# Optimization experiments

Hardware: AMD Instinct MI355X
Metric: run time of the kernel (lower is better)

Reference implementation:

```python
import jax, jax.numpy as jnp
import numpy as np

PATCHES = 196
HEADS = 12


def build_attention_mask(patches, memory_tokens_list, extension=False):
    """Additive mask: masked entries -inf, allowed entries 0. Shape (1, Sq, Skv)."""
    class_tokens = len(memory_tokens_list) + 1
    input_tokens = patches + class_tokens
    total_tokens = input_tokens + sum(memory_tokens_list)
    mask = np.zeros((1, input_tokens, total_tokens), dtype=np.float32)
    mask[:, :, patches + 1:] = -np.inf
    prev = 0
    for i, mtok in enumerate(memory_tokens_list):
        ct = patches + 1 + i
        ms = input_tokens + prev
        me = ms + mtok
        if extension:
            mask[:, ct:, ct] = 0.0
            mask[:, ct:, ms:me] = 0.0
        else:
            mask[:, ct, ct] = 0.0
            mask[:, ct, ms:me] = 0.0
        prev += mtok
    return mask


def setup_inputs() -> dict:
    key = jax.random.key(0)
    ks = jax.random.split(key, 5)
    B, Sq, D, M = 64, PATCHES + 2, 768, 8  # 1 base class token + 1 memory class token
    std = 0.02
    return {
        "hidden_states": jax.random.normal(ks[0], (B, Sq, D), jnp.float32),
        "memory": jax.random.normal(ks[1], (1, M, D), jnp.float32) * std,
        "Wq": jax.random.normal(ks[2], (D, D), jnp.float32) * std,
        "bq": jnp.zeros((D,), jnp.float32),
        "Wk": jax.random.normal(ks[3], (D, D), jnp.float32) * std,
        "bk": jnp.zeros((D,), jnp.float32),
        "Wv": jax.random.normal(ks[4], (D, D), jnp.float32) * std,
        "bv": jnp.zeros((D,), jnp.float32),
    }


def _split_heads(x, heads):
    B, S, D = x.shape
    return x.reshape(B, S, heads, D // heads)  # bshd


def reference(hidden_states, memory, Wq, bq, Wk, bk, Wv, bv):
    B, Sq, D = hidden_states.shape
    M = memory.shape[1]
    head_dim = D // HEADS
    scale = 1.0 / jnp.sqrt(jnp.asarray(head_dim, hidden_states.dtype))
    # static additive mask (1, Sq, Skv)
    mask = jnp.asarray(build_attention_mask(PATCHES, [M]))

    with_memory = jnp.concatenate(
        [hidden_states, jnp.broadcast_to(memory, (B, M, D))], axis=1)  # (B, Skv, D)

    q = _split_heads(hidden_states @ Wq + bq, HEADS)  # (B,Sq,H,dh)
    k = _split_heads(with_memory @ Wk + bk, HEADS)    # (B,Skv,H,dh)
    v = _split_heads(with_memory @ Wv + bv, HEADS)

    scores = jnp.einsum("bqhd,bkhd->bhqk", q, k) * scale + mask[:, None]  # (B,H,Sq,Skv)
    probs = jax.nn.softmax(scores, axis=-1)  # dropout is identity in eval
    ctx = jnp.einsum("bhqk,bkhd->bqhd", probs, v)
    return ctx.reshape(B, Sq, D)
```

## Files before the change

### kernel.cpp

```cpp
#include <hip/hip_runtime.h>

typedef __attribute__((ext_vector_type(8))) short bf16x8;
typedef __attribute__((ext_vector_type(4))) float f32x4;
typedef __attribute__((ext_vector_type(4))) unsigned int u32x4;

#define NB 64
#define SQ 198
#define SKV 206
#define DM 768
#define NH 12
#define NROWS (NB * SKV)
#define NCOL 2304

static __device__ __forceinline__ unsigned short f2b(float f) {
  union { float f; unsigned u; } v; v.f = f;
  unsigned r = v.u + 0x7FFFu + ((v.u >> 16) & 1u);
  return (unsigned short)(r >> 16);
}

typedef const __attribute__((address_space(1))) unsigned int g_u32;
typedef __attribute__((address_space(3))) unsigned int l_u32;
static __device__ __forceinline__ void gload_lds16(const void* g, void* l) {
  __builtin_amdgcn_global_load_lds((g_u32*)g, (l_u32*)l, 16, 0, 0);
}

__global__ __launch_bounds__(256) void k_conv_x(const float* __restrict__ hid,
                                                const float* __restrict__ mem,
                                                unsigned short* __restrict__ xkv) {
  int idx = (blockIdx.x * 256 + threadIdx.x) * 8;
  int r = idx / DM;
  int c = idx - r * DM;
  int b = r / SKV, s = r - b * SKV;
  const float* src = (s < SQ) ? (hid + (b * SQ + s) * DM + c)
                              : (mem + (s - SQ) * DM + c);
  float4 v0 = ((const float4*)src)[0];
  float4 v1 = ((const float4*)src)[1];
  unsigned w0 = f2b(v0.x) | ((unsigned)f2b(v0.y) << 16);
  unsigned w1 = f2b(v0.z) | ((unsigned)f2b(v0.w) << 16);
  unsigned w2 = f2b(v1.x) | ((unsigned)f2b(v1.y) << 16);
  unsigned w3 = f2b(v1.z) | ((unsigned)f2b(v1.w) << 16);
  u32x4 o = {w0, w1, w2, w3};
  *(u32x4*)(xkv + idx) = o;
}

__global__ __launch_bounds__(256) void k_conv_w(const float* __restrict__ Wq,
                                                const float* __restrict__ Wk,
                                                const float* __restrict__ Wv,
                                                unsigned short* __restrict__ wt) {
  __shared__ float L[64][65];
  int w = blockIdx.z;
  int n0 = blockIdx.x * 64, k0 = blockIdx.y * 64;
  const float* W = (w == 0) ? Wq : (w == 1) ? Wk : Wv;
  int tid = threadIdx.x;
#pragma unroll
  for (int i = 0; i < 16; ++i) {
    int idx = i * 256 + tid;
    int lr = idx >> 6, lc = idx & 63;
    L[lr][lc] = W[(k0 + lr) * DM + n0 + lc];
  }
  __syncthreads();
  unsigned short* dst = wt + w * DM * DM;
#pragma unroll
  for (int o = 0; o < 2; ++o) {
    int gi = o * 256 + tid;
    int rn = gi >> 3, g = gi & 7;
    unsigned wrd[4];
#pragma unroll
    for (int jj = 0; jj < 4; ++jj) {
      float f0 = L[g * 8 + jj * 2 + 0][rn];
      float f1 = L[g * 8 + jj * 2 + 1][rn];
      wrd[jj] = f2b(f0) | ((unsigned)f2b(f1) << 16);
    }
    u32x4 o4 = {wrd[0], wrd[1], wrd[2], wrd[3]};
    *(u32x4*)(dst + (n0 + rn) * DM + k0 + g * 8) = o4;
  }
}

__global__ __launch_bounds__(256, 2) void k_gemm(const unsigned short* __restrict__ xkv,
                                                 const unsigned short* __restrict__ wt,
                                                 const float* __restrict__ bq,
                                                 const float* __restrict__ bk,
                                                 const float* __restrict__ bv,
                                                 unsigned short* __restrict__ cout) {
  __shared__ __align__(16) unsigned char smem[34816];
  int nt = blockIdx.x, mt = blockIdx.y;
  int row0 = mt * 128, col0 = nt * 128;
  int w = nt / 6;
  int colw0 = col0 - w * 768;
  int tid = threadIdx.x, lane = tid & 63, wid = tid >> 6;
  int wr = wid >> 1, wc = wid & 1;
  const unsigned short* wbase = wt + w * DM * DM;

  f32x4 zero = {0.f, 0.f, 0.f, 0.f};
  f32x4 acc[4][4];
#pragma unroll
  for (int i = 0; i < 4; ++i)
#pragma unroll
    for (int j = 0; j < 4; ++j) acc[i][j] = zero;

  const unsigned short* aSrc[4];
  const unsigned short* bSrc[4];
#pragma unroll
  for (int j = 0; j < 4; ++j) {
    int s = (wid * 4 + j) * 64 + lane;
    int r = s >> 3, g = s & 7;
    int gsrc = g ^ (r & 7);
    aSrc[j] = xkv   + (row0 + r)  * DM + gsrc * 8;
    bSrc[j] = wbase + (colw0 + r) * DM + gsrc * 8;
  }

  for (int ks = 0; ks < 12; ++ks) {
    int k0 = ks * 64;
    if (ks) __syncthreads();
#pragma unroll
    for (int j = 0; j < 4; ++j) {
      gload_lds16(aSrc[j] + k0, smem + (wid * 4 + j) * 1024);
      gload_lds16(bSrc[j] + k0, smem + 16384 + (wid * 4 + j) * 1024);
    }
    __syncthreads();
#pragma unroll
    for (int kk = 0; kk < 2; ++kk) {
      bf16x8 a[4], b[4];
      int kbyte = (kk * 32 + ((lane >> 4) * 8)) * 2;
#pragma unroll
      for (int mi = 0; mi < 4; ++mi) {
        int rr = wr * 64 + mi * 16 + (lane & 15);
        a[mi] = *(const bf16x8*)(smem + ((rr * 128 + kbyte) ^ ((rr & 7) << 4)));
      }
#pragma unroll
      for (int ni = 0; ni < 4; ++ni) {
        int rr = wc * 64 + ni * 16 + (lane & 15);
        b[ni] = *(const bf16x8*)(smem + 16384 + ((rr * 128 + kbyte) ^ ((rr & 7) << 4)));
      }
#pragma unroll
      for (int mi = 0; mi < 4; ++mi)
#pragma unroll
        for (int ni = 0; ni < 4; ++ni)
          acc[mi][ni] = __builtin_amdgcn_mfma_f32_16x16x32_bf16(a[mi], b[ni], acc[mi][ni], 0, 0, 0);
    }
  }

  const float* bias = (w == 0) ? bq : (w == 1) ? bk : bv;
  float bb[4];
#pragma unroll
  for (int ni = 0; ni < 4; ++ni) bb[ni] = bias[colw0 + wc * 64 + ni * 16 + (lane & 15)];

  __syncthreads();
#pragma unroll
  for (int mi = 0; mi < 4; ++mi)
#pragma unroll
    for (int ni = 0; ni < 4; ++ni)
#pragma unroll
      for (int r = 0; r < 4; ++r) {
        int row = wr * 64 + mi * 16 + (lane >> 4) * 4 + r;
        int col = wc * 64 + ni * 16 + (lane & 15);
        *(unsigned short*)(smem + row * 272 + col * 2) = f2b(acc[mi][ni][r] + bb[ni]);
      }
  __syncthreads();
#pragma unroll
  for (int it = 0; it < 8; ++it) {
    int gi = it * 256 + tid;
    int row = gi >> 4, g = gi & 15;
    u32x4 v = *(const u32x4*)(smem + row * 272 + g * 16);
    *(u32x4*)(cout + (row0 + row) * NCOL + col0 + g * 8) = v;
  }
}

static __device__ __forceinline__ int vt_off(int row, int col) {
  return row * 416 + ((col * 2) ^ (((row >> 3) & 1) << 4));
}

__global__ __launch_bounds__(256, 3) void k_attn(const unsigned short* __restrict__ cqkv,
                                                 float* __restrict__ out) {
  __shared__ __align__(16) unsigned short Ksh[208 * 64];
  __shared__ __align__(16) unsigned char  VtB[64 * 416];
  int bh = blockIdx.x;
  int b = bh / NH, h = bh - b * NH;
  int tid = threadIdx.x, lane = tid & 63, wid = tid >> 6;
  int g = lane >> 4, l = lane & 15;
  const unsigned short* Cb = cqkv + (b * SKV) * NCOL + h * 64;

  if (tid < 64) *(unsigned*)(VtB + vt_off(tid, 206)) = 0u;
  for (int i = tid; i < 208 * 8; i += 256) {
    int row = i >> 3, gg = i & 7;
    int srow = (row < SKV) ? row : (SKV - 1);
    u32x4 v = *(const u32x4*)(Cb + srow * NCOL + 768 + gg * 8);
    *(u32x4*)((unsigned char*)Ksh + ((row * 128 + gg * 16) ^ ((row & 7) << 4))) = v;
  }
  for (int i = tid; i < 206 * 8; i += 256) {
    int key = i >> 3, gg = i & 7;
    u32x4 v = *(const u32x4*)(Cb + key * NCOL + 1536 + gg * 8);
    union { u32x4 v4; unsigned short e[8]; } u; u.v4 = v;
#pragma unroll
    for (int j = 0; j < 8; ++j)
      *(unsigned short*)(VtB + vt_off(gg * 8 + j, key)) = u.e[j];
  }
  __syncthreads();

  const float scale = 0.125f;
  f32x4 zero4 = {0.f, 0.f, 0.f, 0.f};
  int srcA = ((g & 1) << 5) + l;
  int srcB = srcA + 16;
  bool hiHalf = (g >= 2);

  for (int qt = wid; qt < 13; qt += 4) {
    int qr = qt * 16 + l;
    int qld = qr > 197 ? 197 : qr;
    const unsigned short* qp = Cb + qld * NCOL + g * 8;
    bf16x8 qa0 = *(const bf16x8*)qp;
    bf16x8 qa1 = *(const bf16x8*)(qp + 32);

    f32x4 sc[13];
#pragma unroll
    for (int nt = 0; nt < 13; ++nt) sc[nt] = zero4;
#pragma unroll
    for (int nt = 0; nt < 13; ++nt) {
      int key = nt * 16 + l;
      int rb = key * 128, sw = (key & 7) << 4, kb = g * 16;
      bf16x8 kb0 = *(const bf16x8*)((const unsigned char*)Ksh + rb + (kb ^ sw));
      bf16x8 kb1 = *(const bf16x8*)((const unsigned char*)Ksh + rb + ((kb + 64) ^ sw));
      sc[nt] = __builtin_amdgcn_mfma_f32_16x16x32_bf16(kb0, qa0, sc[nt], 0, 0, 0);
      sc[nt] = __builtin_amdgcn_mfma_f32_16x16x32_bf16(kb1, qa1, sc[nt], 0, 0, 0);
    }

    float mx = -1e30f;
#pragma unroll
    for (int nt = 0; nt < 13; ++nt)
#pragma unroll
      for (int r = 0; r < 4; ++r) {
        int key = nt * 16 + g * 4 + r;
        float s = sc[nt][r] * scale;
        bool ok = (key < 197 || qr == 197) && (key < SKV);
        s = ok ? s : -1e30f;
        sc[nt][r] = s;
        mx = fmaxf(mx, s);
      }
    mx = fmaxf(mx, __shfl_xor(mx, 16));
    mx = fmaxf(mx, __shfl_xor(mx, 32));
    float sum = 0.f;
#pragma unroll
    for (int nt = 0; nt < 13; ++nt)
#pragma unroll
      for (int r = 0; r < 4; ++r) {
        float p = __expf(sc[nt][r] - mx);
        sc[nt][r] = p;
        sum += p;
      }
    sum += __shfl_xor(sum, 16);
    sum += __shfl_xor(sum, 32);
    float inv = 1.0f / sum;

    unsigned pk0[13], pk1[13];
#pragma unroll
    for (int nt = 0; nt < 13; ++nt) {
      asm("v_cvt_pk_bf16_f32 %0, %1, %2" : "=v"(pk0[nt]) : "v"(sc[nt][0]), "v"(sc[nt][1]));
      asm("v_cvt_pk_bf16_f32 %0, %1, %2" : "=v"(pk1[nt]) : "v"(sc[nt][2]), "v"(sc[nt][3]));
    }

    f32x4 ctx[4];
#pragma unroll
    for (int dt = 0; dt < 4; ++dt) ctx[dt] = zero4;
#pragma unroll
    for (int c = 0; c < 7; ++c) {
      union { unsigned w[4]; bf16x8 v; } pa;
      if (c < 6) {
        int n0 = 2 * c, n1 = 2 * c + 1;
        unsigned a0 = (unsigned)__shfl((int)pk0[n0], srcA), b0 = (unsigned)__shfl((int)pk0[n1], srcA);
        unsigned a1 = (unsigned)__shfl((int)pk1[n0], srcA), b1 = (unsigned)__shfl((int)pk1[n1], srcA);
        unsigned a2 = (unsigned)__shfl((int)pk0[n0], srcB), b2 = (unsigned)__shfl((int)pk0[n1], srcB);
        unsigned a3 = (unsigned)__shfl((int)pk1[n0], srcB), b3 = (unsigned)__shfl((int)pk1[n1], srcB);
        pa.w[0] = hiHalf ? b0 : a0;
        pa.w[1] = hiHalf ? b1 : a1;
        pa.w[2] = hiHalf ? b2 : a2;
        pa.w[3] = hiHalf ? b3 : a3;
      } else {
        unsigned a0 = (unsigned)__shfl((int)pk0[12], srcA);
        unsigned a1 = (unsigned)__shfl((int)pk1[12], srcA);
        unsigned a2 = (unsigned)__shfl((int)pk0[12], srcB);
        unsigned a3 = (unsigned)__shfl((int)pk1[12], srcB);
        pa.w[0] = hiHalf ? 0u : a0;
        pa.w[1] = hiHalf ? 0u : a1;
        pa.w[2] = hiHalf ? 0u : a2;
        pa.w[3] = hiHalf ? 0u : a3;
      }
      int colb = c * 32 + g * 8;
      if (c == 6 && hiHalf) colb = 0;
#pragma unroll
      for (int dt = 0; dt < 4; ++dt) {
        bf16x8 vb = *(const bf16x8*)(VtB + vt_off(dt * 16 + l, colb));
        ctx[dt] = __builtin_amdgcn_mfma_f32_16x16x32_bf16(pa.v, vb, ctx[dt], 0, 0, 0);
      }
    }

    float invr[4];
#pragma unroll
    for (int r = 0; r < 4; ++r) invr[r] = __shfl(inv, g * 4 + r);
#pragma unroll
    for (int dt = 0; dt < 4; ++dt)
#pragma unroll
      for (int r = 0; r < 4; ++r) {
        int qo = qt * 16 + g * 4 + r;
        if (qo < SQ)
          out[(b * SQ + qo) * DM + h * 64 + dt * 16 + l] = ctx[dt][r] * invr[r];
      }
  }
}

extern "C" void kernel_launch(void* const* d_in, const int* in_sizes, int n_in,
                              void* d_out, int out_size, void* d_ws, size_t ws_size,
                              hipStream_t stream) {
  const float* hid = (const float*)d_in[0];
  const float* mem = (const float*)d_in[1];
  const float* Wq  = (const float*)d_in[2];
  const float* bq  = (const float*)d_in[3];
  const float* Wk  = (const float*)d_in[4];
  const float* bk  = (const float*)d_in[5];
  const float* Wv  = (const float*)d_in[6];
  const float* bv  = (const float*)d_in[7];
  float* out = (float*)d_out;

  unsigned short* xkv  = (unsigned short*)d_ws;
  unsigned short* wt   = xkv + NROWS * DM;
  unsigned short* cbuf = wt + 3 * DM * DM;

  k_conv_x<<<dim3(NROWS * DM / 8 / 256), 256, 0, stream>>>(hid, mem, xkv);
  k_conv_w<<<dim3(12, 12, 3), 256, 0, stream>>>(Wq, Wk, Wv, wt);
  k_gemm<<<dim3(18, 103), 256, 0, stream>>>(xkv, wt, bq, bk, bv, cbuf);
  k_attn<<<dim3(NB * NH), 256, 0, stream>>>(cbuf, out);
}
```

Before: 105.7 us.

## Restructure QKV GEMM into 256x256 tiles with 4-stage async LDS pipeline

The QKV projection GEMM moves from 128x128 tiles with 256 threads and a single-buffered K loop to 256x256 tiles with 512 threads. A 4-deep ring of 32-wide K slices is filled with global_load_lds, and synchronisation uses vmcnt waits plus raw barriers so that loads overlap MFMA work. Blocks are remapped with an XCD-aware swizzle for L2 locality, and s_setprio is raised around the MFMA bursts. The aim is more data reuse per tile and less load stall. In exchange it uses 128KB of LDS, so only one block fits per CU, and the last row tile is partial, which needs row clamping and guarded stores.

```diff
diff --git a/kernel.cpp b/kernel.cpp
--- a/kernel.cpp
+++ b/kernel.cpp
@@ -76,93 +76,118 @@
   }
 }
 
-__global__ __launch_bounds__(256, 2) void k_gemm(const unsigned short* __restrict__ xkv,
+__global__ __launch_bounds__(512, 2) void k_gemm(const unsigned short* __restrict__ xkv,
                                                  const unsigned short* __restrict__ wt,
                                                  const float* __restrict__ bq,
                                                  const float* __restrict__ bk,
                                                  const float* __restrict__ bv,
                                                  unsigned short* __restrict__ cout) {
-  __shared__ __align__(16) unsigned char smem[34816];
-  int nt = blockIdx.x, mt = blockIdx.y;
-  int row0 = mt * 128, col0 = nt * 128;
-  int w = nt / 6;
-  int colw0 = col0 - w * 768;
+  __shared__ __align__(16) unsigned char smem[131072];
+  int o = blockIdx.x, xcd = o & 7, rest = o >> 3;
+  int sid = (xcd < 4 ? xcd * 59 : 236 + (xcd - 4) * 58) + rest;
+  int mtile = sid / 9, ntile = sid - mtile * 9;
+  int row0 = mtile * 256, col0 = ntile * 256;
+  int w = ntile / 3;
+  int colw0 = (ntile - w * 3) * 256;
   int tid = threadIdx.x, lane = tid & 63, wid = tid >> 6;
-  int wr = wid >> 1, wc = wid & 1;
+  int wm = wid >> 2, wn = wid & 3;
+  int l = lane & 15, gq = lane >> 4;
   const unsigned short* wbase = wt + w * DM * DM;
 
+  int sr = tid >> 2, pg = tid & 3, sg = pg ^ (sr & 3);
+  int arow0 = row0 + sr;        if (arow0 > NROWS - 1) arow0 = NROWS - 1;
+  int arow1 = row0 + 128 + sr;  if (arow1 > NROWS - 1) arow1 = NROWS - 1;
+  const unsigned short* aP0 = xkv + arow0 * DM + sg * 8;
+  const unsigned short* aP1 = xkv + arow1 * DM + sg * 8;
+  const unsigned short* bP0 = wbase + (colw0 + sr) * DM + sg * 8;
+  const unsigned short* bP1 = wbase + (colw0 + 128 + sr) * DM + sg * 8;
+  int ldsW = wid * 1024;
+
   f32x4 zero = {0.f, 0.f, 0.f, 0.f};
-  f32x4 acc[4][4];
-#pragma unroll
-  for (int i = 0; i < 4; ++i)
+  f32x4 acc[8][4];
+#pragma unroll
+  for (int i = 0; i < 8; ++i)
 #pragma unroll
     for (int j = 0; j < 4; ++j) acc[i][j] = zero;
 
-  const unsigned short* aSrc[4];
-  const unsigned short* bSrc[4];
-#pragma unroll
-  for (int j = 0; j < 4; ++j) {
-    int s = (wid * 4 + j) * 64 + lane;
-    int r = s >> 3, g = s & 7;
-    int gsrc = g ^ (r & 7);
-    aSrc[j] = xkv   + (row0 + r)  * DM + gsrc * 8;
-    bSrc[j] = wbase + (colw0 + r) * DM + gsrc * 8;
-  }
-
-  for (int ks = 0; ks < 12; ++ks) {
-    int k0 = ks * 64;
-    if (ks) __syncthreads();
-#pragma unroll
-    for (int j = 0; j < 4; ++j) {
-      gload_lds16(aSrc[j] + k0, smem + (wid * 4 + j) * 1024);
-      gload_lds16(bSrc[j] + k0, smem + 16384 + (wid * 4 + j) * 1024);
-    }
-    __syncthreads();
-#pragma unroll
-    for (int kk = 0; kk < 2; ++kk) {
-      bf16x8 a[4], b[4];
-      int kbyte = (kk * 32 + ((lane >> 4) * 8)) * 2;
-#pragma unroll
-      for (int mi = 0; mi < 4; ++mi) {
-        int rr = wr * 64 + mi * 16 + (lane & 15);
-        a[mi] = *(const bf16x8*)(smem + ((rr * 128 + kbyte) ^ ((rr & 7) << 4)));
-      }
-#pragma unroll
-      for (int ni = 0; ni < 4; ++ni) {
-        int rr = wc * 64 + ni * 16 + (lane & 15);
-        b[ni] = *(const bf16x8*)(smem + 16384 + ((rr * 128 + kbyte) ^ ((rr & 7) << 4)));
-      }
-#pragma unroll
-      for (int mi = 0; mi < 4; ++mi)
-#pragma unroll
-        for (int ni = 0; ni < 4; ++ni)
-          acc[mi][ni] = __builtin_amdgcn_mfma_f32_16x16x32_bf16(a[mi], b[ni], acc[mi][ni], 0, 0, 0);
-    }
-  }
+#pragma unroll
+  for (int p = 0; p < 3; ++p) {
+    gload_lds16(aP0 + p * 32, smem + p * 16384 + ldsW);
+    gload_lds16(aP1 + p * 32, smem + p * 16384 + 8192 + ldsW);
+    gload_lds16(bP0 + p * 32, smem + 65536 + p * 16384 + ldsW);
+    gload_lds16(bP1 + p * 32, smem + 65536 + p * 16384 + 8192 + ldsW);
+  }
+
+  int swx = (gq * 16) ^ ((l & 3) << 4);
+  int aRd = (wm * 128 + l) * 64 + swx;
+  int bRd = 65536 + (wn * 64 + l) * 64 + swx;
+
+  auto doTile = [&](int t) {
+    int bo = (t & 3) * 16384;
+    bf16x8 a[8], b[4];
+#pragma unroll
+    for (int mi = 0; mi < 8; ++mi) a[mi] = *(const bf16x8*)(smem + bo + aRd + mi * 1024);
+#pragma unroll
+    for (int ni = 0; ni < 4; ++ni) b[ni] = *(const bf16x8*)(smem + bo + bRd + ni * 1024);
+    __builtin_amdgcn_s_setprio(1);
+#pragma unroll
+    for (int mi = 0; mi < 8; ++mi)
+#pragma unroll
+      for (int ni = 0; ni < 4; ++ni)
+        acc[mi][ni] = __builtin_amdgcn_mfma_f32_16x16x32_bf16(a[mi], b[ni], acc[mi][ni], 0, 0, 0);
+    __builtin_amdgcn_s_setprio(0);
+  };
+
+#pragma unroll 1
+  for (int t = 0; t < 22; ++t) {
+    asm volatile("s_waitcnt vmcnt(8)" ::: "memory");
+    __builtin_amdgcn_s_barrier();
+    asm volatile("" ::: "memory");
+    if (t < 21) {
+      int io = ((t + 3) & 3) * 16384;
+      int kI = (t + 3) * 32;
+      gload_lds16(aP0 + kI, smem + io + ldsW);
+      gload_lds16(aP1 + kI, smem + io + 8192 + ldsW);
+      gload_lds16(bP0 + kI, smem + 65536 + io + ldsW);
+      gload_lds16(bP1 + kI, smem + 65536 + io + 8192 + ldsW);
+    }
+    doTile(t);
+  }
+  asm volatile("s_waitcnt vmcnt(4)" ::: "memory");
+  __builtin_amdgcn_s_barrier();
+  asm volatile("" ::: "memory");
+  doTile(22);
+  asm volatile("s_waitcnt vmcnt(0)" ::: "memory");
+  __builtin_amdgcn_s_barrier();
+  asm volatile("" ::: "memory");
+  doTile(23);
 
   const float* bias = (w == 0) ? bq : (w == 1) ? bk : bv;
   float bb[4];
 #pragma unroll
-  for (int ni = 0; ni < 4; ++ni) bb[ni] = bias[colw0 + wc * 64 + ni * 16 + (lane & 15)];
+  for (int ni = 0; ni < 4; ++ni) bb[ni] = bias[colw0 + wn * 64 + ni * 16 + l];
 
   __syncthreads();
 #pragma unroll
-  for (int mi = 0; mi < 4; ++mi)
+  for (int mi = 0; mi < 8; ++mi)
 #pragma unroll
     for (int ni = 0; ni < 4; ++ni)
 #pragma unroll
-      for (int r = 0; r < 4; ++r) {
-        int row = wr * 64 + mi * 16 + (lane >> 4) * 4 + r;
-        int col = wc * 64 + ni * 16 + (lane & 15);
-        *(unsigned short*)(smem + row * 272 + col * 2) = f2b(acc[mi][ni][r] + bb[ni]);
+      for (int rr = 0; rr < 4; ++rr) {
+        int row = wm * 128 + mi * 16 + gq * 4 + rr;
+        int col = wn * 64 + ni * 16 + l;
+        *(unsigned short*)(smem + row * 512 + ((col * 2) ^ ((row & 7) << 4))) =
+            f2b(acc[mi][ni][rr] + bb[ni]);
       }
   __syncthreads();
 #pragma unroll
-  for (int it = 0; it < 8; ++it) {
-    int gi = it * 256 + tid;
-    int row = gi >> 4, g = gi & 15;
-    u32x4 v = *(const u32x4*)(smem + row * 272 + g * 16);
-    *(u32x4*)(cout + (row0 + row) * NCOL + col0 + g * 8) = v;
+  for (int it = 0; it < 16; ++it) {
+    int gi = it * 512 + tid;
+    int row = gi >> 5, gran = gi & 31;
+    if (row0 + row < NROWS) {
+      u32x4 v = *(const u32x4*)(smem + row * 512 + ((gran * 16) ^ ((row & 7) << 4)));
+      *(u32x4*)(cout + (row0 + row) * NCOL + col0 + gran * 8) = v;
+    }
   }
 }
 
@@ -325,6 +350,6 @@
 
   k_conv_x<<<dim3(NROWS * DM / 8 / 256), 256, 0, stream>>>(hid, mem, xkv);
   k_conv_w<<<dim3(12, 12, 3), 256, 0, stream>>>(Wq, Wk, Wv, wt);
-  k_gemm<<<dim3(18, 103), 256, 0, stream>>>(xkv, wt, bq, bk, bv, cbuf);
+  k_gemm<<<dim3(468), 512, 0, stream>>>(xkv, wt, bq, bk, bv, cbuf);
   k_attn<<<dim3(NB * NH), 256, 0, stream>>>(cbuf, out);
 }
```

Measured after the change: 105.0 us. About the same (-0.6%).
